# Kernel optimization log

Measured on AMD Instinct MI355X. Metric: run time of the kernel, lower is better.

Reference implementation:

```python
import jax
import jax.numpy as jnp
from jax import lax
import numpy as np

DIM = 256
WIN = 7


def setup_inputs() -> dict:
    key = jax.random.key(0)
    ks = jax.random.split(key, 7)
    B, C, H, W = 16, DIM, 64, 64
    k = WIN
    return {
        "x": jax.random.normal(ks[0], (B, C, H, W), dtype=jnp.float32),
        "dw_weight": jax.random.normal(ks[1], (C, 1, k, k), dtype=jnp.float32) * 0.1,
        "pw_weight": jax.random.normal(ks[2], (C, C), dtype=jnp.float32) * 0.05,
        "w1": jax.random.normal(ks[3], (C // 4, C), dtype=jnp.float32) * 0.05,
        "b1": jax.random.normal(ks[4], (C // 4,), dtype=jnp.float32) * 0.05,
        "w2": jax.random.normal(ks[5], (C * k * k, C // 4), dtype=jnp.float32) * 0.05,
        "b2": jax.random.normal(ks[6], (C * k * k,), dtype=jnp.float32) * 0.05,
    }


def reference(x, dw_weight, pw_weight, w1, b1, w2, b2):
    B, C, H, W = x.shape
    k = dw_weight.shape[-1]
    pad = k // 2
    # dynamic kernel generator: global avg pool -> 1x1 conv -> GELU -> 1x1 conv
    pooled = x.mean(axis=(2, 3))                                  # [B, C]
    h = jax.nn.gelu(pooled @ w1.T + b1, approximate=False)        # [B, C//4]
    dyn = (h @ w2.T + b2).reshape(B, C, 1, k, k)                  # [B, C, 1, k, k]
    # fuse static depthwise weights with dynamic per-sample weights
    fused = dw_weight[None] + dyn                                  # [B, C, 1, k, k]
    # per-instance depthwise conv via groups = B*C
    x_flat = x.reshape(1, B * C, H, W)
    kern = fused.reshape(B * C, 1, k, k)
    out = lax.conv_general_dilated(
        x_flat, kern,
        window_strides=(1, 1),
        padding=[(pad, pad), (pad, pad)],
        feature_group_count=B * C,
        dimension_numbers=("NCHW", "OIHW", "NCHW"),
    )
    out = out.reshape(B, C, H, W)
    # final 1x1 pointwise conv (no bias)
    return jnp.einsum("bchw,oc->bohw", out, pw_weight)
```

## Files before the change

kernel.cpp:

```cpp
#include <hip/hip_runtime.h>
#include <math.h>
#include <stdint.h>

typedef __attribute__((ext_vector_type(8))) short short8;
typedef __attribute__((ext_vector_type(4))) float f32x4;

#define B_  16
#define C_  256
#define HW_ 4096
#define KK_ 49
#define CR_ 64

__device__ __forceinline__ ushort f2bf(float f) {
    union { float f; uint32_t u; } v; v.f = f;
    uint32_t r = (v.u + 0x7FFFu + ((v.u >> 16) & 1u)) >> 16;
    return (ushort)r;
}

#define GLDS16(gp, lp) __builtin_amdgcn_global_load_lds(\
    (const __attribute__((address_space(1))) uint32_t*)(gp), \
    (__attribute__((address_space(3))) uint32_t*)(lp), 16, 0, 0)
#define GLDS4(gp, lp) __builtin_amdgcn_global_load_lds(\
    (const __attribute__((address_space(1))) uint32_t*)(gp), \
    (__attribute__((address_space(3))) uint32_t*)(lp), 4, 0, 0)

__global__ __launch_bounds__(256) void pool_kernel(const float* __restrict__ x,
                                                   float* __restrict__ pooled) {
    int bc = blockIdx.x;
    const float4* p4 = (const float4*)(x + (size_t)bc * HW_);
    float s = 0.f;
    for (int i = threadIdx.x; i < HW_ / 4; i += 256) {
        float4 v = p4[i];
        s += (v.x + v.y) + (v.z + v.w);
    }
#pragma unroll
    for (int off = 32; off > 0; off >>= 1) s += __shfl_down(s, off);
    __shared__ float red[4];
    if ((threadIdx.x & 63) == 0) red[threadIdx.x >> 6] = s;
    __syncthreads();
    if (threadIdx.x == 0)
        pooled[bc] = (red[0] + red[1] + red[2] + red[3]) * (1.f / HW_);
}

__global__ __launch_bounds__(256) void mlpgenw_kernel(const float* __restrict__ pooled,
                                                      const float* __restrict__ w1,
                                                      const float* __restrict__ b1,
                                                      const float* __restrict__ w2,
                                                      const float* __restrict__ b2,
                                                      const float* __restrict__ dwt,
                                                      float* __restrict__ fused) {
    __shared__ float ps[B_ * C_];
    __shared__ float hs[B_ * CR_];
    const int tid = threadIdx.x;
    for (int i = tid; i < B_ * C_; i += 256) ps[i] = pooled[i];
    __syncthreads();
    for (int v = tid; v < B_ * CR_; v += 256) {
        int b = v >> 6, r = v & 63;
        float acc = b1[r];
        const float* wr = w1 + (size_t)r * C_;
        const float* pb = ps + b * C_;
        for (int c = 0; c < C_; c += 4) {
            float4 wv = *(const float4*)(wr + c);
            acc += pb[c] * wv.x + pb[c + 1] * wv.y + pb[c + 2] * wv.z + pb[c + 3] * wv.w;
        }
        hs[v] = 0.5f * acc * (1.f + erff(acc * 0.70710678118654752f));
    }
    __syncthreads();

    int m = blockIdx.x * 256 + tid;
    float wrow[CR_];
    const float4* w4 = (const float4*)(w2 + (size_t)m * CR_);
#pragma unroll
    for (int i = 0; i < CR_ / 4; i++) {
        float4 v = w4[i];
        wrow[4 * i] = v.x; wrow[4 * i + 1] = v.y;
        wrow[4 * i + 2] = v.z; wrow[4 * i + 3] = v.w;
    }
    float base = b2[m] + dwt[m];
    for (int b = 0; b < B_; b++) {
        float acc = base;
        const float* hb = hs + b * CR_;
#pragma unroll
        for (int r = 0; r < CR_; r++) acc += hb[r] * wrow[r];
        fused[(size_t)b * (C_ * KK_) + m] = acc;
    }
}

__global__ __launch_bounds__(256) void prep_kernel(const float* __restrict__ pw,
                                                   ushort* __restrict__ Pa) {
    int idx = blockIdx.x * 256 + threadIdx.x;
    int o = idx >> 8, c = idx & 255;
    Pa[(size_t)(((o >> 4) * 32) + (c >> 3)) * 128 + (o & 15) * 8 + (c & 7)] = f2bf(pw[idx]);
}

__global__ __launch_bounds__(512, 6) void dw_kernel(const float* __restrict__ x,
                                                    const float* __restrict__ fused,
                                                    ushort* __restrict__ Ug) {
    __shared__ __align__(16) float xs[8 * 22 * 72];
    ushort* Us = (ushort*)xs;

    const int strip = blockIdx.x;
    const int cb    = blockIdx.y;
    const int b     = blockIdx.z;
    const int tid   = threadIdx.x;
    const int wid   = tid >> 6;
    const int lane  = tid & 63;
    const int c0    = cb * 8;
    const int r0    = strip * 16;

    {
        const float* xp = x + (((size_t)(b * C_ + c0 + wid)) << 12);
        float* xd = xs + wid * 1584;
#pragma unroll
        for (int row = 0; row < 22; row++) {
            int gr = r0 + row - 3;
            if ((unsigned)gr < 64u) {
                GLDS4(xp + (gr << 6) + lane, xd + row * 72 + 4);
            } else if (lane < 36) {
                xd[row * 72 + 2 * lane] = 0.f;
                xd[row * 72 + 2 * lane + 1] = 0.f;
            }
        }
        for (int j = lane; j < 176; j += 64) {
            int row = j >> 3, e = j & 7;
            int col = (e < 4) ? e : (64 + e);
            xd[row * 72 + col] = 0.f;
        }
    }

    float wk[49];
    {
        const float* fp = fused + (((size_t)b * C_) + c0 + wid) * KK_;
        float v = (lane < KK_) ? fp[lane] : 0.f;
        int vi = __float_as_int(v);
#pragma unroll
        for (int t = 0; t < 49; t++) {
            wk[t] = __int_as_float(__builtin_amdgcn_readlane(vi, t));
            asm volatile("" : "+s"(wk[t]));
        }
    }
    __syncthreads();

    const int cg = lane & 15;
    const int rg = lane >> 4;
    float acc[4][4];
#pragma unroll
    for (int ro = 0; ro < 4; ro++)
#pragma unroll
        for (int co = 0; co < 4; co++) acc[ro][co] = 0.f;

    const float* xbase = xs + wid * 1584 + (rg * 4) * 72 + cg * 4;
#pragma unroll
    for (int rr = 0; rr < 10; rr++) {
        float xr[12];
        *(float4*)&xr[0] = *(const float4*)(xbase + rr * 72);
        *(float4*)&xr[4] = *(const float4*)(xbase + rr * 72 + 4);
        *(float4*)&xr[8] = *(const float4*)(xbase + rr * 72 + 8);
        const int olo = (rr - 6 < 0) ? 0 : rr - 6;
        const int ohi = (rr < 3) ? rr : 3;
#pragma unroll
        for (int ro = olo; ro <= ohi; ro++) {
            const int ki = rr - ro;
#pragma unroll
            for (int j = 0; j < 7; j++) {
#pragma unroll
                for (int co = 0; co < 4; co++)
                    acc[ro][co] = fmaf(xr[co + 1 + j], wk[ki * 7 + j], acc[ro][co]);
            }
        }
    }
    __syncthreads();

#pragma unroll
    for (int ro = 0; ro < 4; ro++) {
#pragma unroll
        for (int co = 0; co < 4; co++) {
            int o = rg * 4 + ro;
            int c = cg * 4 + co;
            Us[(o * 4 + (c >> 4)) * 128 + (c & 15) * 8 + wid] = f2bf(acc[ro][co]);
        }
    }
    __syncthreads();

    for (int t = tid; t < 1024; t += 512) {
        int q = t >> 4, part = t & 15;
        int o = q >> 2, cgrp = q & 3;
        size_t e = ((((size_t)b * 256) + (size_t)((r0 + o) * 4 + cgrp)) * 32 + cb) * 128
                   + (size_t)part * 8;
        *(uint4*)(Ug + e) = *(const uint4*)(Us + q * 128 + part * 8);
    }
}

__global__ __launch_bounds__(256, 2) void pw_kernel(const ushort* __restrict__ Pa,
                                                    const ushort* __restrict__ Ug,
                                                    float* __restrict__ Y) {
    __shared__ ushort As[2][8192];
    __shared__ ushort Bs[2][4096];
    const int pb   = blockIdx.x;
    const int b    = blockIdx.y;
    const int tid  = threadIdx.x;
    const int w    = tid >> 6;
    const int lane = tid & 63;
    const int oi   = lane & 15;
    const int kq   = lane >> 4;

    f32x4 acc[4][8];
#pragma unroll
    for (int mi = 0; mi < 4; mi++)
#pragma unroll
        for (int ni = 0; ni < 8; ni++)
            acc[mi][ni] = (f32x4){0.f, 0.f, 0.f, 0.f};

    const size_t ubase = (((size_t)b * 256) + (size_t)pb * 8) * 32 * 128;

#define STAGE(BUF, KB0)                                                          \
    for (int q = w; q < 24; q += 4) {                                            \
        const ushort* src; ushort* dst;                                          \
        if (q < 16) { src = Pa + ((size_t)q * 32 + (KB0)) * 128;                 \
                      dst = &As[BUF][q * 512]; }                                 \
        else { int pg = q - 16;                                                  \
               src = Ug + ubase + ((size_t)pg * 32 + (KB0)) * 128;               \
               dst = &Bs[BUF][pg * 512]; }                                       \
        GLDS16(src + lane * 8, dst);                                             \
    }

    STAGE(0, 0)

#pragma unroll
    for (int ki = 0; ki < 8; ki++) {
        const int buf = ki & 1;
        if (ki < 7) {
            STAGE(buf ^ 1, (ki + 1) * 4)
            asm volatile("s_waitcnt vmcnt(6)" ::: "memory");
        } else {
            asm volatile("s_waitcnt vmcnt(0)" ::: "memory");
        }
        __builtin_amdgcn_s_barrier();
        __builtin_amdgcn_sched_barrier(0);

        short8 af[4], bf[8];
#pragma unroll
        for (int mi = 0; mi < 4; mi++)
            af[mi] = *(const short8*)&As[buf][(w * 4 + mi) * 512 + kq * 128 + oi * 8];
#pragma unroll
        for (int ni = 0; ni < 8; ni++)
            bf[ni] = *(const short8*)&Bs[buf][ni * 512 + kq * 128 + oi * 8];
#pragma unroll
        for (int mi = 0; mi < 4; mi++)
#pragma unroll
            for (int ni = 0; ni < 8; ni++)
                acc[mi][ni] = __builtin_amdgcn_mfma_f32_16x16x32_bf16(
                    bf[ni], af[mi], acc[mi][ni], 0, 0, 0);

        __builtin_amdgcn_s_barrier();
        __builtin_amdgcn_sched_barrier(0);
    }

    float* yb = Y + ((size_t)b << 20);
    const int p0 = pb * 128;
#pragma unroll
    for (int mi = 0; mi < 4; mi++) {
        const int o = w * 64 + mi * 16 + oi;
#pragma unroll
        for (int ni = 0; ni < 8; ni++) {
            const int p = p0 + ni * 16 + kq * 4;
            *(float4*)(yb + (size_t)o * HW_ + p) = *(float4*)&acc[mi][ni];
        }
    }
#undef STAGE
}

extern "C" void kernel_launch(void* const* d_in, const int* in_sizes, int n_in,
                              void* d_out, int out_size, void* d_ws, size_t ws_size,
                              hipStream_t stream) {
    const float* x  = (const float*)d_in[0];
    const float* dw = (const float*)d_in[1];
    const float* pw = (const float*)d_in[2];
    const float* w1 = (const float*)d_in[3];
    const float* b1 = (const float*)d_in[4];
    const float* w2 = (const float*)d_in[5];
    const float* b2 = (const float*)d_in[6];
    float* out = (float*)d_out;

    char* ws = (char*)d_ws;
    float*  pooled = (float*)(ws);
    float*  fused  = (float*)(ws + 16384);
    ushort* Pa     = (ushort*)(ws + 819200);
    ushort* Ug     = (ushort*)(ws + 1048576);

    hipLaunchKernelGGL(pool_kernel,    dim3(B_ * C_), dim3(256), 0, stream, x, pooled);
    hipLaunchKernelGGL(mlpgenw_kernel, dim3(49), dim3(256), 0, stream,
                       pooled, w1, b1, w2, b2, dw, fused);
    hipLaunchKernelGGL(prep_kernel,    dim3(256), dim3(256), 0, stream, pw, Pa);
    hipLaunchKernelGGL(dw_kernel,      dim3(4, 32, B_), dim3(512), 0, stream, x, fused, Ug);
    hipLaunchKernelGGL(pw_kernel,      dim3(32, B_), dim3(256), 0, stream, Pa, Ug, out);
}
```

Before: 116.4 us.

## Fuse depthwise conv and pointwise GEMM into one kernel without intermediate buffer

Replaces the separate depthwise kernel and bf16 pointwise GEMM kernel with a single kernel. Each block owns a 4-row band of one sample and loops over input channels 16 at a time. It double-buffers the x halo tiles in LDS, writes the depthwise results as bf16 into a small LDS tile, and feeds MFMA every two iterations with pointwise weight fragments read straight from global memory. This removes the global write and re-read of the intermediate tensor and one launch. In exchange it re-reads more x halo rows (10 rows per 4 output rows), waits on all loads each iteration, runs one 512-thread block per sample band (256 blocks), and writes the output with scalar stores.

```diff
diff --git a/kernel.cpp b/kernel.cpp
--- a/kernel.cpp
+++ b/kernel.cpp
@@ -17,9 +17,6 @@
     return (ushort)r;
 }
 
-#define GLDS16(gp, lp) __builtin_amdgcn_global_load_lds(\
-    (const __attribute__((address_space(1))) uint32_t*)(gp), \
-    (__attribute__((address_space(3))) uint32_t*)(lp), 16, 0, 0)
 #define GLDS4(gp, lp) __builtin_amdgcn_global_load_lds(\
     (const __attribute__((address_space(1))) uint32_t*)(gp), \
     (__attribute__((address_space(3))) uint32_t*)(lp), 4, 0, 0)
@@ -90,181 +87,141 @@
                                                    ushort* __restrict__ Pa) {
     int idx = blockIdx.x * 256 + threadIdx.x;
     int o = idx >> 8, c = idx & 255;
-    Pa[(size_t)(((o >> 4) * 32) + (c >> 3)) * 128 + (o & 15) * 8 + (c & 7)] = f2bf(pw[idx]);
-}
-
-__global__ __launch_bounds__(512, 6) void dw_kernel(const float* __restrict__ x,
-                                                    const float* __restrict__ fused,
-                                                    ushort* __restrict__ Ug) {
-    __shared__ __align__(16) float xs[8 * 22 * 72];
-    ushort* Us = (ushort*)xs;
-
-    const int strip = blockIdx.x;
-    const int cb    = blockIdx.y;
-    const int b     = blockIdx.z;
-    const int tid   = threadIdx.x;
-    const int wid   = tid >> 6;
-    const int lane  = tid & 63;
-    const int c0    = cb * 8;
-    const int r0    = strip * 16;
-
-    {
-        const float* xp = x + (((size_t)(b * C_ + c0 + wid)) << 12);
-        float* xd = xs + wid * 1584;
-#pragma unroll
-        for (int row = 0; row < 22; row++) {
-            int gr = r0 + row - 3;
-            if ((unsigned)gr < 64u) {
-                GLDS4(xp + (gr << 6) + lane, xd + row * 72 + 4);
-            } else if (lane < 36) {
-                xd[row * 72 + 2 * lane] = 0.f;
-                xd[row * 72 + 2 * lane + 1] = 0.f;
-            }
-        }
-        for (int j = lane; j < 176; j += 64) {
-            int row = j >> 3, e = j & 7;
-            int col = (e < 4) ? e : (64 + e);
-            xd[row * 72 + col] = 0.f;
-        }
-    }
-
-    float wk[49];
-    {
-        const float* fp = fused + (((size_t)b * C_) + c0 + wid) * KK_;
-        float v = (lane < KK_) ? fp[lane] : 0.f;
-        int vi = __float_as_int(v);
-#pragma unroll
-        for (int t = 0; t < 49; t++) {
-            wk[t] = __int_as_float(__builtin_amdgcn_readlane(vi, t));
-            asm volatile("" : "+s"(wk[t]));
-        }
-    }
-    __syncthreads();
-
-    const int cg = lane & 15;
-    const int rg = lane >> 4;
-    float acc[4][4];
-#pragma unroll
-    for (int ro = 0; ro < 4; ro++)
-#pragma unroll
-        for (int co = 0; co < 4; co++) acc[ro][co] = 0.f;
-
-    const float* xbase = xs + wid * 1584 + (rg * 4) * 72 + cg * 4;
-#pragma unroll
-    for (int rr = 0; rr < 10; rr++) {
-        float xr[12];
-        *(float4*)&xr[0] = *(const float4*)(xbase + rr * 72);
-        *(float4*)&xr[4] = *(const float4*)(xbase + rr * 72 + 4);
-        *(float4*)&xr[8] = *(const float4*)(xbase + rr * 72 + 8);
-        const int olo = (rr - 6 < 0) ? 0 : rr - 6;
-        const int ohi = (rr < 3) ? rr : 3;
-#pragma unroll
-        for (int ro = olo; ro <= ohi; ro++) {
-            const int ki = rr - ro;
-#pragma unroll
-            for (int j = 0; j < 7; j++) {
-#pragma unroll
-                for (int co = 0; co < 4; co++)
-                    acc[ro][co] = fmaf(xr[co + 1 + j], wk[ki * 7 + j], acc[ro][co]);
-            }
-        }
-    }
-    __syncthreads();
-
-#pragma unroll
-    for (int ro = 0; ro < 4; ro++) {
-#pragma unroll
-        for (int co = 0; co < 4; co++) {
-            int o = rg * 4 + ro;
-            int c = cg * 4 + co;
-            Us[(o * 4 + (c >> 4)) * 128 + (c & 15) * 8 + wid] = f2bf(acc[ro][co]);
-        }
-    }
-    __syncthreads();
-
-    for (int t = tid; t < 1024; t += 512) {
-        int q = t >> 4, part = t & 15;
-        int o = q >> 2, cgrp = q & 3;
-        size_t e = ((((size_t)b * 256) + (size_t)((r0 + o) * 4 + cgrp)) * 32 + cb) * 128
-                   + (size_t)part * 8;
-        *(uint4*)(Ug + e) = *(const uint4*)(Us + q * 128 + part * 8);
-    }
-}
-
-__global__ __launch_bounds__(256, 2) void pw_kernel(const ushort* __restrict__ Pa,
-                                                    const ushort* __restrict__ Ug,
-                                                    float* __restrict__ Y) {
-    __shared__ ushort As[2][8192];
-    __shared__ ushort Bs[2][4096];
-    const int pb   = blockIdx.x;
+    size_t e = (size_t)((((c >> 5) * 16 + (o >> 4)) * 4 + ((c >> 3) & 3)) * 128)
+             + (o & 15) * 8 + (c & 7);
+    Pa[e] = f2bf(pw[idx]);
+}
+
+__global__ __launch_bounds__(512, 2) void dwpw_kernel(const float* __restrict__ x,
+                                                      const float* __restrict__ fused,
+                                                      const ushort* __restrict__ Pa,
+                                                      float* __restrict__ Y) {
+    __shared__ __align__(16) float  xs[2][16][10][72];
+    __shared__ __align__(16) ushort Us[16][16][40];
+
+    const int band = blockIdx.x;
     const int b    = blockIdx.y;
     const int tid  = threadIdx.x;
-    const int w    = tid >> 6;
+    const int wid  = tid >> 6;
     const int lane = tid & 63;
+    const int r0   = band * 4;
+    const int ow   = wid >> 2;
+    const int pq   = wid & 3;
+    const int cg   = lane & 15;
+    const int rg   = lane >> 4;
     const int oi   = lane & 15;
     const int kq   = lane >> 4;
 
-    f32x4 acc[4][8];
-#pragma unroll
-    for (int mi = 0; mi < 4; mi++)
-#pragma unroll
-        for (int ni = 0; ni < 8; ni++)
-            acc[mi][ni] = (f32x4){0.f, 0.f, 0.f, 0.f};
-
-    const size_t ubase = (((size_t)b * 256) + (size_t)pb * 8) * 32 * 128;
-
-#define STAGE(BUF, KB0)                                                          \
-    for (int q = w; q < 24; q += 4) {                                            \
-        const ushort* src; ushort* dst;                                          \
-        if (q < 16) { src = Pa + ((size_t)q * 32 + (KB0)) * 128;                 \
-                      dst = &As[BUF][q * 512]; }                                 \
-        else { int pg = q - 16;                                                  \
-               src = Ug + ubase + ((size_t)pg * 32 + (KB0)) * 128;               \
-               dst = &Bs[BUF][pg * 512]; }                                       \
-        GLDS16(src + lane * 8, dst);                                             \
-    }
-
-    STAGE(0, 0)
-
-#pragma unroll
-    for (int ki = 0; ki < 8; ki++) {
-        const int buf = ki & 1;
-        if (ki < 7) {
-            STAGE(buf ^ 1, (ki + 1) * 4)
-            asm volatile("s_waitcnt vmcnt(6)" ::: "memory");
-        } else {
-            asm volatile("s_waitcnt vmcnt(0)" ::: "memory");
-        }
-        __builtin_amdgcn_s_barrier();
-        __builtin_amdgcn_sched_barrier(0);
-
-        short8 af[4], bf[8];
-#pragma unroll
-        for (int mi = 0; mi < 4; mi++)
-            af[mi] = *(const short8*)&As[buf][(w * 4 + mi) * 512 + kq * 128 + oi * 8];
-#pragma unroll
-        for (int ni = 0; ni < 8; ni++)
-            bf[ni] = *(const short8*)&Bs[buf][ni * 512 + kq * 128 + oi * 8];
-#pragma unroll
-        for (int mi = 0; mi < 4; mi++)
-#pragma unroll
-            for (int ni = 0; ni < 8; ni++)
-                acc[mi][ni] = __builtin_amdgcn_mfma_f32_16x16x32_bf16(
-                    bf[ni], af[mi], acc[mi][ni], 0, 0, 0);
-
-        __builtin_amdgcn_s_barrier();
-        __builtin_amdgcn_sched_barrier(0);
-    }
-
-    float* yb = Y + ((size_t)b << 20);
-    const int p0 = pb * 128;
-#pragma unroll
-    for (int mi = 0; mi < 4; mi++) {
-        const int o = w * 64 + mi * 16 + oi;
-#pragma unroll
-        for (int ni = 0; ni < 8; ni++) {
-            const int p = p0 + ni * 16 + kq * 4;
-            *(float4*)(yb + (size_t)o * HW_ + p) = *(float4*)&acc[mi][ni];
+    {
+        float* xf = &xs[0][0][0][0];
+        for (int i = tid; i < 2 * 16 * 10 * 72; i += 512) xf[i] = 0.f;
+    }
+    __syncthreads();
+
+#define STAGE(IT)                                                                  \
+    {                                                                              \
+        _Pragma("unroll")                                                          \
+        for (int q = 0; q < 2; q++) {                                              \
+            const int slot = wid + 8 * q;                                          \
+            const int ch   = (IT) * 16 + slot;                                     \
+            const float* xp = x + (((size_t)b * C_ + ch) << 12);                   \
+            _Pragma("unroll")                                                      \
+            for (int row = 0; row < 10; row++) {                                   \
+                int gr = r0 + row - 3;                                             \
+                if ((unsigned)gr < 64u)                                            \
+                    GLDS4(xp + (gr << 6) + lane, &xs[(IT) & 1][slot][row][4]);     \
+            }                                                                      \
+        }                                                                          \
+    }
+
+    f32x4 acc[8][4];
+#pragma unroll
+    for (int i = 0; i < 8; i++)
+#pragma unroll
+        for (int j = 0; j < 4; j++) acc[i][j] = (f32x4){0.f, 0.f, 0.f, 0.f};
+
+    STAGE(0)
+
+    for (int it = 0; it < 16; it++) {
+        asm volatile("s_waitcnt vmcnt(0)" ::: "memory");
+        const int buf = it & 1;
+        const bool mf = (it & 1) != 0;
+
+        short8 afrag[8];
+        if (mf) {
+            const int kb = it >> 1;
+#pragma unroll
+            for (int j = 0; j < 8; j++) {
+                const int ob = ow * 8 + j;
+                afrag[j] = *(const short8*)(Pa
+                    + (size_t)(((kb * 16 + ob) * 4 + kq) * 128) + oi * 8);
+            }
+        }
+        if (it < 15) STAGE(it + 1)
+
+#pragma unroll
+        for (int s = 0; s < 2; s++) {
+            const int slot = wid + 8 * s;
+            const int ch   = it * 16 + slot;
+            const float* fp = fused + ((size_t)b * C_ + ch) * KK_;
+            float v = (lane < KK_) ? fp[lane] : 0.f;
+            int vi = __float_as_int(v);
+            float wk[49];
+#pragma unroll
+            for (int t = 0; t < 49; t++) {
+                wk[t] = __int_as_float(__builtin_amdgcn_readlane(vi, t));
+                asm volatile("" : "+s"(wk[t]));
+            }
+            float a4[4] = {0.f, 0.f, 0.f, 0.f};
+            const float* xb = &xs[buf][slot][0][cg * 4];
+#pragma unroll
+            for (int ki = 0; ki < 7; ki++) {
+                float xr[12];
+                const float* rp = xb + (rg + ki) * 72;
+                *(float4*)&xr[0] = *(const float4*)rp;
+                *(float4*)&xr[4] = *(const float4*)(rp + 4);
+                *(float4*)&xr[8] = *(const float4*)(rp + 8);
+#pragma unroll
+                for (int kj = 0; kj < 7; kj++)
+#pragma unroll
+                    for (int co = 0; co < 4; co++)
+                        a4[co] = fmaf(xr[co + 1 + kj], wk[ki * 7 + kj], a4[co]);
+            }
+            const int k = buf * 16 + slot;
+#pragma unroll
+            for (int co = 0; co < 4; co++) {
+                int px = rg * 64 + cg * 4 + co;
+                Us[px >> 4][px & 15][k] = f2bf(a4[co]);
+            }
+        }
+
+        if (mf) {
+            __syncthreads();
+            short8 bfrag[4];
+#pragma unroll
+            for (int j = 0; j < 4; j++)
+                bfrag[j] = *(const short8*)&Us[pq * 4 + j][oi][kq * 8];
+#pragma unroll
+            for (int i = 0; i < 8; i++)
+#pragma unroll
+                for (int j = 0; j < 4; j++)
+                    acc[i][j] = __builtin_amdgcn_mfma_f32_16x16x32_bf16(
+                        afrag[i], bfrag[j], acc[i][j], 0, 0, 0);
+            __syncthreads();
+        }
+    }
+
+    float* yb = Y + ((size_t)b << 20) + band * 256;
+#pragma unroll
+    for (int i = 0; i < 8; i++) {
+#pragma unroll
+        for (int j = 0; j < 4; j++) {
+            const int p = pq * 64 + j * 16 + oi;
+#pragma unroll
+            for (int r = 0; r < 4; r++) {
+                const int o = ow * 128 + i * 16 + kq * 4 + r;
+                yb[(size_t)o * HW_ + p] = acc[i][j][r];
+            }
         }
     }
 #undef STAGE
@@ -286,12 +243,11 @@
     float*  pooled = (float*)(ws);
     float*  fused  = (float*)(ws + 16384);
     ushort* Pa     = (ushort*)(ws + 819200);
-    ushort* Ug     = (ushort*)(ws + 1048576);
 
     hipLaunchKernelGGL(pool_kernel,    dim3(B_ * C_), dim3(256), 0, stream, x, pooled);
     hipLaunchKernelGGL(mlpgenw_kernel, dim3(49), dim3(256), 0, stream,
                        pooled, w1, b1, w2, b2, dw, fused);
     hipLaunchKernelGGL(prep_kernel,    dim3(256), dim3(256), 0, stream, pw, Pa);
-    hipLaunchKernelGGL(dw_kernel,      dim3(4, 32, B_), dim3(512), 0, stream, x, fused, Ug);
-    hipLaunchKernelGGL(pw_kernel,      dim3(32, B_), dim3(256), 0, stream, Pa, Ug, out);
-}
+    hipLaunchKernelGGL(dwpw_kernel,    dim3(16, B_), dim3(512), 0, stream,
+                       x, fused, Pa, out);
+}
```

After: 147.8 us. 1.27x slower.

## Shrink pointwise GEMM tile, read weights from global, plain loads in depthwise

Applied to the files above, without the earlier changes.

The pointwise GEMM kernel now uses a 64-pixel tile, so the grid doubles and occupancy is raised to 4 blocks per SM. It stages only the activation tile in LDS and reads the bf16 weight fragments straight from global/L2, with the weight prep layout reordered to suit. The depthwise kernel swaps global_load_lds for ordinary loads into a 3-float padded layout, which cuts the per-thread row read from 12 to 10 floats, and its occupancy hint drops to 4. These changes aim to improve occupancy and parallelism, at the cost of more global/L2 traffic for the weights and a single-buffer wait (vmcnt(0)) each k-step.

```diff
diff --git a/kernel.cpp b/kernel.cpp
--- a/kernel.cpp
+++ b/kernel.cpp
@@ -20,9 +20,6 @@
 #define GLDS16(gp, lp) __builtin_amdgcn_global_load_lds(\
     (const __attribute__((address_space(1))) uint32_t*)(gp), \
     (__attribute__((address_space(3))) uint32_t*)(lp), 16, 0, 0)
-#define GLDS4(gp, lp) __builtin_amdgcn_global_load_lds(\
-    (const __attribute__((address_space(1))) uint32_t*)(gp), \
-    (__attribute__((address_space(3))) uint32_t*)(lp), 4, 0, 0)
 
 __global__ __launch_bounds__(256) void pool_kernel(const float* __restrict__ x,
                                                    float* __restrict__ pooled) {
@@ -90,10 +87,12 @@
                                                    ushort* __restrict__ Pa) {
     int idx = blockIdx.x * 256 + threadIdx.x;
     int o = idx >> 8, c = idx & 255;
-    Pa[(size_t)(((o >> 4) * 32) + (c >> 3)) * 128 + (o & 15) * 8 + (c & 7)] = f2bf(pw[idx]);
-}
-
-__global__ __launch_bounds__(512, 6) void dw_kernel(const float* __restrict__ x,
+    size_t e = (size_t)((((c >> 5) * 16 + (o >> 4)) * 4 + ((c >> 3) & 3)) * 128)
+             + (o & 15) * 8 + (c & 7);
+    Pa[e] = f2bf(pw[idx]);
+}
+
+__global__ __launch_bounds__(512, 4) void dw_kernel(const float* __restrict__ x,
                                                     const float* __restrict__ fused,
                                                     ushort* __restrict__ Ug) {
     __shared__ __align__(16) float xs[8 * 22 * 72];
@@ -114,16 +113,13 @@
 #pragma unroll
         for (int row = 0; row < 22; row++) {
             int gr = r0 + row - 3;
-            if ((unsigned)gr < 64u) {
-                GLDS4(xp + (gr << 6) + lane, xd + row * 72 + 4);
-            } else if (lane < 36) {
-                xd[row * 72 + 2 * lane] = 0.f;
-                xd[row * 72 + 2 * lane + 1] = 0.f;
-            }
+            float v = 0.f;
+            if ((unsigned)gr < 64u) v = xp[(gr << 6) + lane];
+            xd[row * 72 + 3 + lane] = v;
         }
         for (int j = lane; j < 176; j += 64) {
             int row = j >> 3, e = j & 7;
-            int col = (e < 4) ? e : (64 + e);
+            int col = (e < 3) ? e : (64 + e);
             xd[row * 72 + col] = 0.f;
         }
     }
@@ -152,10 +148,10 @@
     const float* xbase = xs + wid * 1584 + (rg * 4) * 72 + cg * 4;
 #pragma unroll
     for (int rr = 0; rr < 10; rr++) {
-        float xr[12];
+        float xr[10];
         *(float4*)&xr[0] = *(const float4*)(xbase + rr * 72);
         *(float4*)&xr[4] = *(const float4*)(xbase + rr * 72 + 4);
-        *(float4*)&xr[8] = *(const float4*)(xbase + rr * 72 + 8);
+        *(float2*)&xr[8] = *(const float2*)(xbase + rr * 72 + 8);
         const int olo = (rr - 6 < 0) ? 0 : rr - 6;
         const int ohi = (rr < 3) ? rr : 3;
 #pragma unroll
@@ -165,7 +161,7 @@
             for (int j = 0; j < 7; j++) {
 #pragma unroll
                 for (int co = 0; co < 4; co++)
-                    acc[ro][co] = fmaf(xr[co + 1 + j], wk[ki * 7 + j], acc[ro][co]);
+                    acc[ro][co] = fmaf(xr[co + j], wk[ki * 7 + j], acc[ro][co]);
             }
         }
     }
@@ -191,83 +187,68 @@
     }
 }
 
-__global__ __launch_bounds__(256, 2) void pw_kernel(const ushort* __restrict__ Pa,
+__global__ __launch_bounds__(256, 4) void pw_kernel(const ushort* __restrict__ Pa,
                                                     const ushort* __restrict__ Ug,
                                                     float* __restrict__ Y) {
-    __shared__ ushort As[2][8192];
-    __shared__ ushort Bs[2][4096];
+    __shared__ ushort Bs[2][2048];
     const int pb   = blockIdx.x;
     const int b    = blockIdx.y;
     const int tid  = threadIdx.x;
-    const int w    = tid >> 6;
+    const int wid  = tid >> 6;
     const int lane = tid & 63;
     const int oi   = lane & 15;
     const int kq   = lane >> 4;
 
-    f32x4 acc[4][8];
+    f32x4 acc[4][4];
 #pragma unroll
     for (int mi = 0; mi < 4; mi++)
 #pragma unroll
-        for (int ni = 0; ni < 8; ni++)
+        for (int ni = 0; ni < 4; ni++)
             acc[mi][ni] = (f32x4){0.f, 0.f, 0.f, 0.f};
 
-    const size_t ubase = (((size_t)b * 256) + (size_t)pb * 8) * 32 * 128;
-
-#define STAGE(BUF, KB0)                                                          \
-    for (int q = w; q < 24; q += 4) {                                            \
-        const ushort* src; ushort* dst;                                          \
-        if (q < 16) { src = Pa + ((size_t)q * 32 + (KB0)) * 128;                 \
-                      dst = &As[BUF][q * 512]; }                                 \
-        else { int pg = q - 16;                                                  \
-               src = Ug + ubase + ((size_t)pg * 32 + (KB0)) * 128;               \
-               dst = &Bs[BUF][pg * 512]; }                                       \
-        GLDS16(src + lane * 8, dst);                                             \
-    }
-
-    STAGE(0, 0)
-
-#pragma unroll
-    for (int ki = 0; ki < 8; ki++) {
-        const int buf = ki & 1;
-        if (ki < 7) {
-            STAGE(buf ^ 1, (ki + 1) * 4)
-            asm volatile("s_waitcnt vmcnt(6)" ::: "memory");
-        } else {
-            asm volatile("s_waitcnt vmcnt(0)" ::: "memory");
-        }
+    const int p16 = pb * 4;
+
+#define STAGEB(KB) GLDS16(Ug + ((((size_t)b * 256 + p16 + wid) * 32 + (KB) * 4) * 128) \
+                              + lane * 8, &Bs[(KB) & 1][wid * 512])
+
+    STAGEB(0);
+
+#pragma unroll
+    for (int kb = 0; kb < 8; kb++) {
+        asm volatile("s_waitcnt vmcnt(0)" ::: "memory");
         __builtin_amdgcn_s_barrier();
-        __builtin_amdgcn_sched_barrier(0);
-
-        short8 af[4], bf[8];
+        if (kb < 7) STAGEB(kb + 1);
+        const int buf = kb & 1;
+
+        short8 af[4], bf[4];
+#pragma unroll
+        for (int mi = 0; mi < 4; mi++) {
+            const int ob = wid * 4 + mi;
+            af[mi] = *(const short8*)(Pa + (size_t)(((kb * 16 + ob) * 4 + kq) * 128) + oi * 8);
+        }
+#pragma unroll
+        for (int ni = 0; ni < 4; ni++)
+            bf[ni] = *(const short8*)&Bs[buf][(ni * 4 + kq) * 128 + oi * 8];
 #pragma unroll
         for (int mi = 0; mi < 4; mi++)
-            af[mi] = *(const short8*)&As[buf][(w * 4 + mi) * 512 + kq * 128 + oi * 8];
-#pragma unroll
-        for (int ni = 0; ni < 8; ni++)
-            bf[ni] = *(const short8*)&Bs[buf][ni * 512 + kq * 128 + oi * 8];
-#pragma unroll
-        for (int mi = 0; mi < 4; mi++)
-#pragma unroll
-            for (int ni = 0; ni < 8; ni++)
+#pragma unroll
+            for (int ni = 0; ni < 4; ni++)
                 acc[mi][ni] = __builtin_amdgcn_mfma_f32_16x16x32_bf16(
                     bf[ni], af[mi], acc[mi][ni], 0, 0, 0);
-
-        __builtin_amdgcn_s_barrier();
-        __builtin_amdgcn_sched_barrier(0);
     }
 
     float* yb = Y + ((size_t)b << 20);
-    const int p0 = pb * 128;
+    const int p0 = pb * 64;
 #pragma unroll
     for (int mi = 0; mi < 4; mi++) {
-        const int o = w * 64 + mi * 16 + oi;
-#pragma unroll
-        for (int ni = 0; ni < 8; ni++) {
+        const int o = wid * 64 + mi * 16 + oi;
+#pragma unroll
+        for (int ni = 0; ni < 4; ni++) {
             const int p = p0 + ni * 16 + kq * 4;
             *(float4*)(yb + (size_t)o * HW_ + p) = *(float4*)&acc[mi][ni];
         }
     }
-#undef STAGE
+#undef STAGEB
 }
 
 extern "C" void kernel_launch(void* const* d_in, const int* in_sizes, int n_in,
@@ -293,5 +274,5 @@
                        pooled, w1, b1, w2, b2, dw, fused);
     hipLaunchKernelGGL(prep_kernel,    dim3(256), dim3(256), 0, stream, pw, Pa);
     hipLaunchKernelGGL(dw_kernel,      dim3(4, 32, B_), dim3(512), 0, stream, x, fused, Ug);
-    hipLaunchKernelGGL(pw_kernel,      dim3(32, B_), dim3(256), 0, stream, Pa, Ug, out);
-}
+    hipLaunchKernelGGL(pw_kernel,      dim3(64, B_), dim3(256), 0, stream, Pa, Ug, out);
+}
```

New measurement: 123.4 us. 6.0% more time.
